# Kernel optimization log

Hardware: AMD Instinct MI355X
Metric: run time of the kernel (lower is better)

## Reference

```python
import jax, jax.numpy as jnp
import numpy as np

P = 16
PW = P // 2 + 1  # 9, rfft width


def setup_inputs() -> dict:
    key = jax.random.key(0)
    ks = jax.random.split(key, 5)
    B, C, H, W = 128, 3, 224, 224
    E = 768
    N = (H // P) * (W // P)  # 196
    return {
        "x": jax.random.normal(ks[0], (B, C, H, W), dtype=jnp.float32),
        "freq_weight_h": jnp.ones((P,), dtype=jnp.float32),
        "freq_weight_w": jnp.ones((PW,), dtype=jnp.float32),
        "proj_w": jax.random.normal(ks[1], (E, C * P * PW), dtype=jnp.float32) * 0.02,
        "proj_b": jnp.zeros((E,), dtype=jnp.float32),
        "cls_token": jax.random.normal(ks[2], (1, 1, E), dtype=jnp.float32),
        "pos_emb": jax.random.normal(ks[3], (1, N + 1, E), dtype=jnp.float32),
    }


def reference(x, freq_weight_h, freq_weight_w, proj_w, proj_b, cls_token, pos_emb):
    B, C, H, W = x.shape
    nH, nW = H // P, W // P
    N = nH * nW
    # unfold into non-overlapping PxP patches: (B, C, N, P, P)
    patches = x.reshape(B, C, nH, P, nW, P).transpose(0, 1, 2, 4, 3, 5)
    patches = patches.reshape(B, C, N, P, P)
    # rfft2 with ortho norm, keep real part: (B, C, N, P, PW)
    x_fft = jnp.fft.rfft2(patches, norm="ortho").real
    # frequency reweighting
    x_fft = x_fft * freq_weight_h[None, None, None, :, None]
    x_fft = x_fft * freq_weight_w[None, None, None, None, :]
    # (B, N, C*P*PW)
    x_flat = x_fft.transpose(0, 2, 1, 3, 4).reshape(B, N, C * P * PW)
    # linear projection to embed_dim
    x_proj = jnp.einsum("bnf,ef->bne", x_flat, proj_w) + proj_b
    # prepend cls token, add position embeddings (dropout is eval/identity)
    cls = jnp.broadcast_to(cls_token, (B, 1, cls_token.shape[-1]))
    out = jnp.concatenate([cls, x_proj], axis=1) + pos_emb
    return out
```

## Files before the change

kernel.cpp:

```cpp
#include <hip/hip_runtime.h>
#include <hip/hip_bf16.h>

typedef __bf16 bf16;
typedef __attribute__((ext_vector_type(8))) __bf16 bf16x8;
typedef __attribute__((ext_vector_type(4))) float floatx4;

#define PP 16
#define PPW 9
#define CFEAT 432
#define EDIM 768
#define KDIM 768
#define NPAT 196
#define NBATCH 128
#define MROWS (NBATCH * NPAT)

#define NB_W 2304
#define NB_CLS 384
#define NB_UNF 9408
#define NB_PREP (NB_W + NB_CLS + NB_UNF)

__device__ inline void gload16(const void* g, void* l) {
  __builtin_amdgcn_global_load_lds(
      (const __attribute__((address_space(1))) void*)g,
      (__attribute__((address_space(3))) void*)l, 16, 0, 0);
}

__global__ __launch_bounds__(256) void prep_kernel(
    const float* __restrict__ x, const float* __restrict__ pw,
    const float* __restrict__ fwh, const float* __restrict__ fww,
    const float* __restrict__ cls, const float* __restrict__ pos,
    bf16* __restrict__ Wb, bf16* __restrict__ A, float* __restrict__ out) {
  const int blk = blockIdx.x;
  const int t = threadIdx.x;

  if (blk >= NB_W + NB_CLS) {
    const int i = (blk - NB_W - NB_CLS) * 256 + t;
    const int w8 = i % 28;
    const int tmp = i / 28;
    const int h = tmp % 224;
    const int tmp2 = tmp / 224;
    const int c = tmp2 % 3;
    const int b = tmp2 / 3;
    const float4 f0 = *reinterpret_cast<const float4*>(x + (size_t)i * 8);
    const float4 f1 = *reinterpret_cast<const float4*>(x + (size_t)i * 8 + 4);
    bf16x8 v;
    v[0] = (bf16)f0.x; v[1] = (bf16)f0.y; v[2] = (bf16)f0.z; v[3] = (bf16)f0.w;
    v[4] = (bf16)f1.x; v[5] = (bf16)f1.y; v[6] = (bf16)f1.z; v[7] = (bf16)f1.w;
    const int row = b * NPAT + (h >> 4) * 14 + (w8 >> 1);
    const int k = c * 256 + (h & 15) * 16 + (w8 & 1) * 8;
    *reinterpret_cast<bf16x8*>(A + (size_t)row * KDIM + k) = v;
  } else if (blk < NB_W) {
    __shared__ float s_pw[144];
    __shared__ float s_fh[16];
    __shared__ float s_fw[9];
    __shared__ float s_cos[16];
    const int e = blk / 3;
    const int c = blk % 3;
    if (t < 144) s_pw[t] = pw[e * CFEAT + c * 144 + t];
    if (t < 16) {
      s_fh[t] = fwh[t];
      s_cos[t] = cosf((float)t * 0.39269908169872414f);
    }
    if (t < 9) s_fw[t] = fww[t];
    __syncthreads();
    const int h = t >> 4, w = t & 15;
    float acc = 0.f;
#pragma unroll
    for (int u = 0; u < 16; ++u) {
      const float fh = s_fh[u];
      const int uh = (u * h) & 15;
#pragma unroll
      for (int v = 0; v < 9; ++v) {
        acc += s_pw[u * 9 + v] * s_fw[v] * s_cos[(uh + v * w) & 15] * fh;
      }
    }
    Wb[e * KDIM + c * 256 + t] = (bf16)(acc * 0.0625f);
  } else {
    const int idx = (blk - NB_W) * 256 + t;
    const int b = idx / 768;
    const int e = idx - b * 768;
    out[(size_t)b * 197 * 768 + e] = cls[e] + pos[e];
  }
}

__global__ __launch_bounds__(256) void gemm_db_kernel(
    const bf16* __restrict__ A, const bf16* __restrict__ Wb,
    const float* __restrict__ pb, const float* __restrict__ pos,
    float* __restrict__ out) {
  __shared__ __align__(16) bf16 sA[2][128 * 32];
  __shared__ __align__(16) bf16 sB[2][128 * 32];

  const int bid = blockIdx.x;
  const int swz = (bid & 7) * 147 + (bid >> 3);
  const int mt = swz / 6;
  const int nt = swz - mt * 6;
  const int t = threadIdx.x;
  const int l = t & 63;
  const int wv = t >> 6;
  const int wm = wv >> 1, wn = wv & 1;
  const int lr = l & 15, lq = l >> 4;

  const int r8 = t >> 2;
  const int r8b = r8 + 64;
  const int sw0 = (r8 ^ (r8 >> 2)) & 3;
  const int sw1 = (r8b ^ (r8b >> 2)) & 3;
  const bf16* gA0 = A + (size_t)(mt * 128 + r8) * KDIM + (((t & 3) ^ sw0) * 8);
  const bf16* gA1 = A + (size_t)(mt * 128 + r8b) * KDIM + (((t & 3) ^ sw1) * 8);
  const bf16* gB0 = Wb + (size_t)(nt * 128 + r8) * KDIM + (((t & 3) ^ sw0) * 8);
  const bf16* gB1 = Wb + (size_t)(nt * 128 + r8b) * KDIM + (((t & 3) ^ sw1) * 8);
  const int lbase = wv * 512;

#define STAGE(buf, kts)                              \
  do {                                               \
    const int ko = (kts)*32;                         \
    gload16(gA0 + ko, &sA[buf][lbase]);              \
    gload16(gA1 + ko, &sA[buf][2048 + lbase]);       \
    gload16(gB0 + ko, &sB[buf][lbase]);              \
    gload16(gB1 + ko, &sB[buf][2048 + lbase]);       \
  } while (0)

  floatx4 acc[4][4];
#pragma unroll
  for (int i = 0; i < 4; ++i)
#pragma unroll
    for (int j = 0; j < 4; ++j) acc[i][j] = (floatx4){0.f, 0.f, 0.f, 0.f};

#define COMPUTE(buf)                                                         \
  do {                                                                       \
    bf16x8 af[4], bfr[4];                                                    \
    _Pragma("unroll") for (int mi = 0; mi < 4; ++mi) {                       \
      const int r = wm * 64 + mi * 16 + lr;                                  \
      const int qp = lq ^ ((r ^ (r >> 2)) & 3);                              \
      af[mi] = *reinterpret_cast<const bf16x8*>(&sA[buf][r * 32 + qp * 8]);  \
    }                                                                        \
    _Pragma("unroll") for (int ni = 0; ni < 4; ++ni) {                       \
      const int r = wn * 64 + ni * 16 + lr;                                  \
      const int qp = lq ^ ((r ^ (r >> 2)) & 3);                              \
      bfr[ni] = *reinterpret_cast<const bf16x8*>(&sB[buf][r * 32 + qp * 8]); \
    }                                                                        \
    _Pragma("unroll") for (int mi = 0; mi < 4; ++mi)                         \
        _Pragma("unroll") for (int ni = 0; ni < 4; ++ni) acc[mi][ni] =       \
            __builtin_amdgcn_mfma_f32_16x16x32_bf16(af[mi], bfr[ni],         \
                                                    acc[mi][ni], 0, 0, 0);   \
  } while (0)

  STAGE(0, 0);
  __syncthreads();
  int cur = 0;
  for (int kt = 0; kt < 23; ++kt) {
    STAGE(cur ^ 1, kt + 1);
    COMPUTE(cur);
    __syncthreads();
    cur ^= 1;
  }
  COMPUTE(cur);
#undef STAGE
#undef COMPUTE

  float pbv[4];
#pragma unroll
  for (int ni = 0; ni < 4; ++ni)
    pbv[ni] = pb[nt * 128 + wn * 64 + ni * 16 + lr];

#pragma unroll
  for (int mi = 0; mi < 4; ++mi) {
#pragma unroll
    for (int j = 0; j < 4; ++j) {
      const unsigned m = wm * 64 + mi * 16 + lq * 4 + j;
      const unsigned Rr = mt * 128u + m;
      const unsigned b2 = Rr / 196u;
      const unsigned np2 = Rr - b2 * 196u;
      float* orow = out + ((size_t)b2 * 197 + 1 + np2) * 768;
      const float* prow = pos + (size_t)(1 + np2) * 768;
#pragma unroll
      for (int ni = 0; ni < 4; ++ni) {
        const int e = nt * 128 + wn * 64 + ni * 16 + lr;
        orow[e] = acc[mi][ni][j] + pbv[ni] + prow[e];
      }
    }
  }
}

extern "C" void kernel_launch(void* const* d_in, const int* in_sizes, int n_in,
                              void* d_out, int out_size, void* d_ws,
                              size_t ws_size, hipStream_t stream) {
  const float* x = (const float*)d_in[0];
  const float* fwh = (const float*)d_in[1];
  const float* fww = (const float*)d_in[2];
  const float* proj_w = (const float*)d_in[3];
  const float* proj_b = (const float*)d_in[4];
  const float* cls = (const float*)d_in[5];
  const float* pos = (const float*)d_in[6];
  float* out = (float*)d_out;

  const size_t needW = (size_t)EDIM * KDIM * sizeof(bf16);
  bf16* Wb = (bf16*)d_ws;
  bf16* A = (bf16*)((char*)d_ws + needW);

  prep_kernel<<<NB_PREP, 256, 0, stream>>>(x, proj_w, fwh, fww, cls, pos, Wb,
                                           A, out);
  gemm_db_kernel<<<1176, 256, 0, stream>>>(A, Wb, proj_b, pos, out);
}
```

Baseline: 81.89 us.

## Fuse patch unfolding and bf16 conversion into GEMM A-tile loading

Drops the separate unfold pass that wrote a bf16 patch matrix to workspace. The GEMM now reads fp32 pixels straight from x in registers, converts them to bf16 and stores them into shared memory, overlapping those loads with the MFMA compute of the current buffer. This removes one full write and read of the intermediate activation matrix. In exchange, each x tile is re-read by all 6 N-tiles, the A path uses register staging instead of direct-to-LDS loads, and the XOR swizzle is dropped, which may bring LDS bank conflicts.

```diff
diff --git a/kernel.cpp b/kernel.cpp
--- a/kernel.cpp
+++ b/kernel.cpp
@@ -16,8 +16,6 @@
 
 #define NB_W 2304
 #define NB_CLS 384
-#define NB_UNF 9408
-#define NB_PREP (NB_W + NB_CLS + NB_UNF)
 
 __device__ inline void gload16(const void* g, void* l) {
   __builtin_amdgcn_global_load_lds(
@@ -25,31 +23,14 @@
       (__attribute__((address_space(3))) void*)l, 16, 0, 0);
 }
 
-__global__ __launch_bounds__(256) void prep_kernel(
-    const float* __restrict__ x, const float* __restrict__ pw,
-    const float* __restrict__ fwh, const float* __restrict__ fww,
-    const float* __restrict__ cls, const float* __restrict__ pos,
-    bf16* __restrict__ Wb, bf16* __restrict__ A, float* __restrict__ out) {
+__global__ __launch_bounds__(256) void prep_small(
+    const float* __restrict__ pw, const float* __restrict__ fwh,
+    const float* __restrict__ fww, const float* __restrict__ cls,
+    const float* __restrict__ pos, bf16* __restrict__ Wb,
+    float* __restrict__ out) {
   const int blk = blockIdx.x;
   const int t = threadIdx.x;
-
-  if (blk >= NB_W + NB_CLS) {
-    const int i = (blk - NB_W - NB_CLS) * 256 + t;
-    const int w8 = i % 28;
-    const int tmp = i / 28;
-    const int h = tmp % 224;
-    const int tmp2 = tmp / 224;
-    const int c = tmp2 % 3;
-    const int b = tmp2 / 3;
-    const float4 f0 = *reinterpret_cast<const float4*>(x + (size_t)i * 8);
-    const float4 f1 = *reinterpret_cast<const float4*>(x + (size_t)i * 8 + 4);
-    bf16x8 v;
-    v[0] = (bf16)f0.x; v[1] = (bf16)f0.y; v[2] = (bf16)f0.z; v[3] = (bf16)f0.w;
-    v[4] = (bf16)f1.x; v[5] = (bf16)f1.y; v[6] = (bf16)f1.z; v[7] = (bf16)f1.w;
-    const int row = b * NPAT + (h >> 4) * 14 + (w8 >> 1);
-    const int k = c * 256 + (h & 15) * 16 + (w8 & 1) * 8;
-    *reinterpret_cast<bf16x8*>(A + (size_t)row * KDIM + k) = v;
-  } else if (blk < NB_W) {
+  if (blk < NB_W) {
     __shared__ float s_pw[144];
     __shared__ float s_fh[16];
     __shared__ float s_fw[9];
@@ -83,8 +64,8 @@
   }
 }
 
-__global__ __launch_bounds__(256) void gemm_db_kernel(
-    const bf16* __restrict__ A, const bf16* __restrict__ Wb,
+__global__ __launch_bounds__(256) void gemm_fused_kernel(
+    const float* __restrict__ x, const bf16* __restrict__ Wb,
     const float* __restrict__ pb, const float* __restrict__ pos,
     float* __restrict__ out) {
   __shared__ __align__(16) bf16 sA[2][128 * 32];
@@ -100,43 +81,66 @@
   const int wm = wv >> 1, wn = wv & 1;
   const int lr = l & 15, lq = l >> 4;
 
-  const int r8 = t >> 2;
-  const int r8b = r8 + 64;
-  const int sw0 = (r8 ^ (r8 >> 2)) & 3;
-  const int sw1 = (r8b ^ (r8b >> 2)) & 3;
-  const bf16* gA0 = A + (size_t)(mt * 128 + r8) * KDIM + (((t & 3) ^ sw0) * 8);
-  const bf16* gA1 = A + (size_t)(mt * 128 + r8b) * KDIM + (((t & 3) ^ sw1) * 8);
-  const bf16* gB0 = Wb + (size_t)(nt * 128 + r8) * KDIM + (((t & 3) ^ sw0) * 8);
-  const bf16* gB1 = Wb + (size_t)(nt * 128 + r8b) * KDIM + (((t & 3) ^ sw1) * 8);
+  const int r = t >> 1, half = t & 1;
+  const int R = mt * 128 + r;
+  const int bb = R / 196, np = R - bb * 196;
+  const int ph = np / 14, pwc = np - ph * 14;
+  const float* xbase =
+      x + ((size_t)(bb * 3) * 224 + ph * 16 + half) * 224 + pwc * 16;
+
+  const bf16* gB0 = Wb + (size_t)(nt * 128 + (t >> 2)) * KDIM + (t & 3) * 8;
+  const bf16* gB1 = gB0 + (size_t)64 * KDIM;
   const int lbase = wv * 512;
 
-#define STAGE(buf, kts)                              \
+  floatx4 acc[4][4];
+#pragma unroll
+  for (int i = 0; i < 4; ++i)
+#pragma unroll
+    for (int j = 0; j < 4; ++j) acc[i][j] = (floatx4){0.f, 0.f, 0.f, 0.f};
+
+#define KOFF(kt) ((((kt) >> 3) * 50176) + ((((kt)*2) & 15) * 224))
+
+#define LOADX(kt, p0, p1, p2, p3)                               \
+  do {                                                          \
+    const float* src = xbase + KOFF(kt);                        \
+    p0 = *reinterpret_cast<const float4*>(src);                 \
+    p1 = *reinterpret_cast<const float4*>(src + 4);             \
+    p2 = *reinterpret_cast<const float4*>(src + 8);             \
+    p3 = *reinterpret_cast<const float4*>(src + 12);            \
+  } while (0)
+
+#define WRITEA(buf, p0, p1, p2, p3)                                \
+  do {                                                             \
+    bf16x8 a0, a1;                                                 \
+    a0[0] = (bf16)p0.x; a0[1] = (bf16)p0.y;                        \
+    a0[2] = (bf16)p0.z; a0[3] = (bf16)p0.w;                        \
+    a0[4] = (bf16)p1.x; a0[5] = (bf16)p1.y;                        \
+    a0[6] = (bf16)p1.z; a0[7] = (bf16)p1.w;                        \
+    a1[0] = (bf16)p2.x; a1[1] = (bf16)p2.y;                        \
+    a1[2] = (bf16)p2.z; a1[3] = (bf16)p2.w;                        \
+    a1[4] = (bf16)p3.x; a1[5] = (bf16)p3.y;                        \
+    a1[6] = (bf16)p3.z; a1[7] = (bf16)p3.w;                        \
+    *reinterpret_cast<bf16x8*>(&sA[buf][r * 32 + half * 16]) = a0; \
+    *reinterpret_cast<bf16x8*>(&sA[buf][r * 32 + half * 16 + 8]) = a1; \
+  } while (0)
+
+#define STAGEB(buf, kts)                             \
   do {                                               \
     const int ko = (kts)*32;                         \
-    gload16(gA0 + ko, &sA[buf][lbase]);              \
-    gload16(gA1 + ko, &sA[buf][2048 + lbase]);       \
     gload16(gB0 + ko, &sB[buf][lbase]);              \
     gload16(gB1 + ko, &sB[buf][2048 + lbase]);       \
   } while (0)
-
-  floatx4 acc[4][4];
-#pragma unroll
-  for (int i = 0; i < 4; ++i)
-#pragma unroll
-    for (int j = 0; j < 4; ++j) acc[i][j] = (floatx4){0.f, 0.f, 0.f, 0.f};
 
 #define COMPUTE(buf)                                                         \
   do {                                                                       \
     bf16x8 af[4], bfr[4];                                                    \
     _Pragma("unroll") for (int mi = 0; mi < 4; ++mi) {                       \
-      const int r = wm * 64 + mi * 16 + lr;                                  \
-      const int qp = lq ^ ((r ^ (r >> 2)) & 3);                              \
-      af[mi] = *reinterpret_cast<const bf16x8*>(&sA[buf][r * 32 + qp * 8]);  \
+      const int rr = wm * 64 + mi * 16 + lr;                                 \
+      af[mi] = *reinterpret_cast<const bf16x8*>(&sA[buf][rr * 32 + lq * 8]); \
     }                                                                        \
     _Pragma("unroll") for (int ni = 0; ni < 4; ++ni) {                       \
-      const int r = wn * 64 + ni * 16 + lr;                                  \
-      const int qp = lq ^ ((r ^ (r >> 2)) & 3);                              \
-      bfr[ni] = *reinterpret_cast<const bf16x8*>(&sB[buf][r * 32 + qp * 8]); \
+      const int rr = wn * 64 + ni * 16 + lr;                                 \
+      bfr[ni] = *reinterpret_cast<const bf16x8*>(&sB[buf][rr * 32 + lq * 8]);\
     }                                                                        \
     _Pragma("unroll") for (int mi = 0; mi < 4; ++mi)                         \
         _Pragma("unroll") for (int ni = 0; ni < 4; ++ni) acc[mi][ni] =       \
@@ -144,17 +148,29 @@
                                                     acc[mi][ni], 0, 0, 0);   \
   } while (0)
 
-  STAGE(0, 0);
-  __syncthreads();
+  {
+    float4 p0, p1, p2, p3;
+    LOADX(0, p0, p1, p2, p3);
+    STAGEB(0, 0);
+    WRITEA(0, p0, p1, p2, p3);
+    __syncthreads();
+  }
+
   int cur = 0;
   for (int kt = 0; kt < 23; ++kt) {
-    STAGE(cur ^ 1, kt + 1);
+    float4 p0, p1, p2, p3;
+    LOADX(kt + 1, p0, p1, p2, p3);
+    STAGEB(cur ^ 1, kt + 1);
     COMPUTE(cur);
+    WRITEA(cur ^ 1, p0, p1, p2, p3);
     __syncthreads();
     cur ^= 1;
   }
   COMPUTE(cur);
-#undef STAGE
+#undef KOFF
+#undef LOADX
+#undef WRITEA
+#undef STAGEB
 #undef COMPUTE
 
   float pbv[4];
@@ -193,11 +209,9 @@
   const float* pos = (const float*)d_in[6];
   float* out = (float*)d_out;
 
-  const size_t needW = (size_t)EDIM * KDIM * sizeof(bf16);
   bf16* Wb = (bf16*)d_ws;
-  bf16* A = (bf16*)((char*)d_ws + needW);
-
-  prep_kernel<<<NB_PREP, 256, 0, stream>>>(x, proj_w, fwh, fww, cls, pos, Wb,
-                                           A, out);
-  gemm_db_kernel<<<1176, 256, 0, stream>>>(A, Wb, proj_b, pos, out);
-}
+
+  prep_small<<<NB_W + NB_CLS, 256, 0, stream>>>(proj_w, fwh, fww, cls, pos,
+                                                Wb, out);
+  gemm_fused_kernel<<<1176, 256, 0, stream>>>(x, Wb, proj_b, pos, out);
+}
```

After: 85.91 us. 1.05x slower.
